# Performance work log

Measured on AMD Instinct MI355X. Metric: run time of the kernel, lower is better.

## Reference

```python
import jax, jax.numpy as jnp
import numpy as np

D_IN, D_HIDDEN, DT_RANK = 768, 16, 48


def setup_inputs() -> dict:
    key = jax.random.key(0)
    ks = jax.random.split(key, 6)
    b, l, d, n, r = 2, 2048, D_IN, D_HIDDEN, DT_RANK
    p = 3 * n + 2 * d + 2 * r  # x_proj output width = 1680
    x = jax.random.normal(ks[0], (b, l, d), jnp.float32)
    z = jax.random.normal(ks[1], (b, d, l), jnp.float32)
    # A_log = log(repeat(arange(1, n+1), 'n -> d n'))
    A_log = jnp.log(jnp.broadcast_to(jnp.arange(1, n + 1, dtype=jnp.float32), (d, n)))
    D = jnp.ones((d,), jnp.float32)
    W_xproj = jax.random.normal(ks[2], (p, d), jnp.float32) / np.sqrt(d)
    W_dt = jax.random.normal(ks[3], (d, r), jnp.float32) / np.sqrt(r)
    # dt bias init: inverse-softplus of dt ~ LogUniform(1e-3, 1e-1)
    dt = jnp.exp(jax.random.uniform(ks[4], (d,)) * (np.log(0.1) - np.log(0.001)) + np.log(0.001))
    dt = jnp.clip(dt, 1e-4)
    b_dt = dt + jnp.log(-jnp.expm1(-dt))
    return dict(x=x, z=z, A_log=A_log, D=D, W_xproj=W_xproj, W_dt=W_dt, b_dt=b_dt)


def reference(x, z, A_log, D, W_xproj, W_dt, b_dt):
    b, l, d = x.shape
    n = A_log.shape[1]
    r = W_dt.shape[1]
    A = -jnp.exp(A_log)                      # (d, n)
    proj = x @ W_xproj.T                     # (b, l, 3n + 2d + 2r)
    Bm = proj[..., :n]                       # (b, l, n)  input matrix B
    Cm = proj[..., 2 * n:3 * n]              # (b, l, n)  output matrix C
    dt = proj[..., 3 * n + 2 * d:3 * n + 2 * d + r]   # (b, l, r)
    # NOTE: source adds dt_proj bias via the Linear AND again via delta_bias -> 2*b_dt
    delta = jax.nn.softplus(dt @ W_dt.T + 2.0 * b_dt)  # (b, l, d)
    dA = jnp.exp(delta[..., None] * A)                  # (b, l, d, n)
    dBu = (delta * x)[..., None] * Bm[:, :, None, :]    # (b, l, d, n)

    def step(h, inp):
        dA_t, dBu_t, C_t = inp
        h = dA_t * h + dBu_t                 # (b, d, n)
        return h, jnp.einsum('bdn,bn->bd', h, C_t)

    h0 = jnp.zeros((b, d, n), x.dtype)
    _, ys = jax.lax.scan(step, h0, (jnp.swapaxes(dA, 0, 1), jnp.swapaxes(dBu, 0, 1), jnp.swapaxes(Cm, 0, 1)))
    y = jnp.swapaxes(ys, 0, 1) + x * D       # (b, l, d)  + skip D*u
    zl = jnp.swapaxes(z, 1, 2)               # z is (b, d, l) -> (b, l, d)
    return y * (zl * jax.nn.sigmoid(zl))     # gate with silu(z)
```

## Files before the change

kernel.cpp:

```cpp
#include <hip/hip_runtime.h>
#include <math.h>

#define BATCH 2
#define LSEQ  2048
#define DIM   768
#define NST   16
#define RDT   48
#define BL    (BATCH*LSEQ)
#define NCHUNK 32
#define CLEN   (LSEQ/NCHUNK)
#define CPAD   68
#define NPACK  (CLEN/4)
#define LP4    (LSEQ/4)
#define L2E    1.4426950408889634f

typedef __attribute__((ext_vector_type(8))) short short8;
typedef __attribute__((ext_vector_type(4))) float float4e;

__device__ __forceinline__ ushort f2bf(float f) {
    union { float f; unsigned u; } v; v.f = f;
    unsigned u = v.u;
    u += 0x7fffu + ((u >> 16) & 1u);
    return (ushort)(u >> 16);
}

template <int CTRL>
__device__ __forceinline__ float dpp_add(float v) {
    const int s = __builtin_amdgcn_update_dpp(__float_as_int(v), __float_as_int(v),
                                              CTRL, 0xF, 0xF, false);
    return v + __int_as_float(s);
}

__global__ __launch_bounds__(256) void pack_kernel(
        const float* __restrict__ x, const float* __restrict__ Wx,
        float* __restrict__ xT, ushort* __restrict__ Wbf) {
    if (blockIdx.y == DIM / 64) {
        const int blk = blockIdx.z * 32 + blockIdx.x;
        for (int idx = blk * 256 + threadIdx.x; idx < 80 * DIM; idx += 64 * 256) {
            const int j = idx / DIM;
            const int k = idx - j * DIM;
            const int row = (j < 16) ? j : ((j < 32) ? (j + 16) : (j + 1552));
            Wbf[idx] = f2bf(Wx[(size_t)row * DIM + k]);
        }
        return;
    }
    __shared__ float tile[64 * 65];
    const int r0 = blockIdx.x * 64;
    const int c0 = blockIdx.y * 64;
    const int b  = blockIdx.z;
    const int tid = threadIdx.x;
    {
        const int c4 = tid & 15, rb = tid >> 4;
        #pragma unroll
        for (int rr = 0; rr < 4; ++rr) {
            const int row = rr * 16 + rb;
            const float4 v = *(const float4*)(x + ((size_t)b * LSEQ + r0 + row) * DIM + c0 + c4 * 4);
            tile[(c4 * 4 + 0) * 65 + row] = v.x;
            tile[(c4 * 4 + 1) * 65 + row] = v.y;
            tile[(c4 * 4 + 2) * 65 + row] = v.z;
            tile[(c4 * 4 + 3) * 65 + row] = v.w;
        }
    }
    __syncthreads();
    {
        const int t4 = tid & 15, dq = tid >> 4;
        #pragma unroll
        for (int pass = 0; pass < 4; ++pass) {
            const int dd = pass * 16 + dq;
            float4 v;
            v.x = tile[dd * 65 + t4 * 4 + 0];
            v.y = tile[dd * 65 + t4 * 4 + 1];
            v.z = tile[dd * 65 + t4 * 4 + 2];
            v.w = tile[dd * 65 + t4 * 4 + 3];
            *(float4*)(xT + ((size_t)b * DIM + c0 + dd) * LSEQ + r0 + t4 * 4) = v;
        }
    }
}

__global__ __launch_bounds__(64) void proj_gemm_kernel(
        const float* __restrict__ x, const ushort* __restrict__ Wbf,
        float* __restrict__ Bpk, float* __restrict__ Cpk,
        float* __restrict__ dtpT) {
    const int m0   = blockIdx.x * 16;
    const int lane = threadIdx.x;
    const int col  = lane & 15;
    const int quad = lane >> 4;

    const float* A  = x + (size_t)(m0 + col) * DIM + quad * 8;
    const short* Bw = (const short*)Wbf;

    float4e acc[5] = {};
    #pragma unroll 4
    for (int kk = 0; kk < 24; ++kk) {
        const float4 a0 = *(const float4*)(A + kk * 32);
        const float4 a1 = *(const float4*)(A + kk * 32 + 4);
        short8 a;
        a[0] = (short)f2bf(a0.x); a[1] = (short)f2bf(a0.y);
        a[2] = (short)f2bf(a0.z); a[3] = (short)f2bf(a0.w);
        a[4] = (short)f2bf(a1.x); a[5] = (short)f2bf(a1.y);
        a[6] = (short)f2bf(a1.z); a[7] = (short)f2bf(a1.w);
        #pragma unroll
        for (int nt = 0; nt < 5; ++nt) {
            const short8 bf = *(const short8*)(Bw + (size_t)(nt * 16 + col) * DIM + kk * 32 + quad * 8);
            acc[nt] = __builtin_amdgcn_mfma_f32_16x16x32_bf16(a, bf, acc[nt], 0, 0, 0);
        }
    }

    const int b  = m0 >> 11;
    const int t0 = m0 & 2047;
    const size_t pk4 = ((size_t)(b * LP4 + (t0 >> 2) + quad)) * NST + col;
    ((float4*)Bpk)[pk4] = *(float4*)&acc[0];
    ((float4*)Cpk)[pk4] = *(float4*)&acc[1];
    #pragma unroll
    for (int nt = 2; nt < 5; ++nt) {
        const int r = (nt - 2) * 16 + col;
        *(float4*)(dtpT + ((size_t)(b * RDT + r)) * LSEQ + t0 + quad * 4) = *(float4*)&acc[nt];
    }
}

__global__ __launch_bounds__(256) void xpose_kernel(
        const float* __restrict__ in, float* __restrict__ out, int R, int C) {
    __shared__ float tile[64 * 65];
    const int r0 = blockIdx.x * 64;
    const int c0 = blockIdx.y * 64;
    const int b  = blockIdx.z;
    const int tid = threadIdx.x;
    {
        const int c4 = tid & 15, rb = tid >> 4;
        #pragma unroll
        for (int rr = 0; rr < 4; ++rr) {
            const int row = rr * 16 + rb;
            const float4 v = *(const float4*)(in + ((size_t)b * R + r0 + row) * C + c0 + c4 * 4);
            tile[(c4 * 4 + 0) * 65 + row] = v.x;
            tile[(c4 * 4 + 1) * 65 + row] = v.y;
            tile[(c4 * 4 + 2) * 65 + row] = v.z;
            tile[(c4 * 4 + 3) * 65 + row] = v.w;
        }
    }
    __syncthreads();
    {
        const int t4 = tid & 15, dq = tid >> 4;
        #pragma unroll
        for (int pass = 0; pass < 4; ++pass) {
            const int dd = pass * 16 + dq;
            float4 v;
            v.x = tile[dd * 65 + t4 * 4 + 0];
            v.y = tile[dd * 65 + t4 * 4 + 1];
            v.z = tile[dd * 65 + t4 * 4 + 2];
            v.w = tile[dd * 65 + t4 * 4 + 3];
            *(float4*)(out + ((size_t)b * C + c0 + dd) * R + r0 + t4 * 4) = v;
        }
    }
}

__global__ __launch_bounds__(512) void scan_kernel(
        const float* __restrict__ xT, const float* __restrict__ z,
        const float* __restrict__ A_log, const float* __restrict__ Dp,
        const float* __restrict__ Bpk, const float* __restrict__ Cpk,
        const float* __restrict__ dtpT, const float* __restrict__ Wdt,
        const float* __restrict__ bdt, float* __restrict__ yT) {
    __shared__ float sdel[NCHUNK * CPAD];
    __shared__ float sdlx[NCHUNK * CPAD];
    __shared__ float sx[NCHUNK * CPAD];
    __shared__ float sP[NCHUNK][NST];
    __shared__ float sq[NCHUNK][NST];
    __shared__ float sw[RDT];

    const int tid = threadIdx.x;
    const int ch = blockIdx.x;
    const int b = ch / DIM;
    const int d = ch % DIM;
    const size_t row = (size_t)ch * LSEQ;

    if (tid < RDT) sw[tid] = Wdt[(size_t)d * RDT + tid];
    const float4 xv4 = ((const float4*)(xT + row))[tid];
    ((float4*)sx)[(tid >> 4) * (CPAD / 4) + (tid & 15)] = xv4;
    __syncthreads();

    {
        const float bb = 2.0f * bdt[d];
        const float* dbase = dtpT + (size_t)b * RDT * LSEQ;
        float4 acc = make_float4(bb, bb, bb, bb);
        #pragma unroll 3
        for (int k4 = 0; k4 < RDT / 4; ++k4) {
            const float4 wv = ((const float4*)sw)[k4];
            #pragma unroll
            for (int j = 0; j < 4; ++j) {
                const int k = k4 * 4 + j;
                const float wk = (j == 0) ? wv.x : (j == 1) ? wv.y : (j == 2) ? wv.z : wv.w;
                const float4 v = ((const float4*)(dbase + (size_t)k * LSEQ))[tid];
                acc.x = fmaf(v.x, wk, acc.x);
                acc.y = fmaf(v.y, wk, acc.y);
                acc.z = fmaf(v.z, wk, acc.z);
                acc.w = fmaf(v.w, wk, acc.w);
            }
        }
        float4 sp;
        sp.x = (acc.x > 20.f) ? acc.x : __logf(1.f + __expf(acc.x));
        sp.y = (acc.y > 20.f) ? acc.y : __logf(1.f + __expf(acc.y));
        sp.z = (acc.z > 20.f) ? acc.z : __logf(1.f + __expf(acc.z));
        sp.w = (acc.w > 20.f) ? acc.w : __logf(1.f + __expf(acc.w));
        const int sidx = (tid >> 4) * (CPAD / 4) + (tid & 15);
        ((float4*)sdel)[sidx] = sp;
        ((float4*)sdlx)[sidx] = make_float4(sp.x * xv4.x, sp.y * xv4.y,
                                            sp.z * xv4.z, sp.w * xv4.w);
    }
    __syncthreads();

    const int g = tid >> 4;
    const int n = tid & 15;
    const float Aln2 = -__expf(A_log[d * NST + n]) * L2E;
    const float4* Bg = (const float4*)Bpk + ((size_t)(b * LP4 + g * NPACK) * NST + n);
    const float4* Cg = (const float4*)Cpk + ((size_t)(b * LP4 + g * NPACK) * NST + n);
    const float* dchunk  = sdel + g * CPAD;
    const float* uxchunk = sdlx + g * CPAD;

    {
        float h = 0.f, Ptot = 1.f;
        float4 Bn_ = Bg[0];
        #pragma unroll 4
        for (int p = 0; p < NPACK; ++p) {
            const float4 B4 = Bn_;
            if (p < NPACK - 1) Bn_ = Bg[(p + 1) * NST];
            const float4 dl = *(const float4*)(dchunk + 4 * p);
            const float4 ux = *(const float4*)(uxchunk + 4 * p);
            const float u0 = ux.x * B4.x, u1 = ux.y * B4.y;
            const float u2 = ux.z * B4.z, u3 = ux.w * B4.w;
            const float e0  = __builtin_amdgcn_exp2f(Aln2 * dl.x);
            const float dA1 = __builtin_amdgcn_exp2f(Aln2 * dl.y);
            const float dA2 = __builtin_amdgcn_exp2f(Aln2 * dl.z);
            const float dA3 = __builtin_amdgcn_exp2f(Aln2 * dl.w);
            float s = u0;
            s = fmaf(dA1, s, u1); s = fmaf(dA2, s, u2); s = fmaf(dA3, s, u3);
            const float E3 = ((e0 * dA1) * (dA2 * dA3));
            h = fmaf(E3, h, s);
            Ptot *= E3;
        }
        sP[g][n] = Ptot;
        sq[g][n] = h;
    }
    __syncthreads();

    {
        float Pc = sP[g][n], qc = sq[g][n];
        #pragma unroll
        for (int s = 1; s < NCHUNK; s <<= 1) {
            float Pp = 1.f, qp = 0.f;
            if (g >= s) { Pp = sP[g - s][n]; qp = sq[g - s][n]; }
            __syncthreads();
            qc = fmaf(Pc, qp, qc);
            Pc *= Pp;
            sP[g][n] = Pc; sq[g][n] = qc;
            __syncthreads();
        }
    }

    {
        float h = (g == 0) ? 0.f : sq[g - 1][n];
        float* ybuf = sdel;
        float4 Bn_ = Bg[0];
        float4 Cn_ = Cg[0];
        #pragma unroll 4
        for (int p = 0; p < NPACK; ++p) {
            const float4 B4 = Bn_, C4 = Cn_;
            if (p < NPACK - 1) { Bn_ = Bg[(p + 1) * NST]; Cn_ = Cg[(p + 1) * NST]; }
            const float4 dl = *(const float4*)(dchunk + 4 * p);
            const float4 ux = *(const float4*)(uxchunk + 4 * p);
            const float u0 = ux.x * B4.x, u1 = ux.y * B4.y;
            const float u2 = ux.z * B4.z, u3 = ux.w * B4.w;
            const float E0  = __builtin_amdgcn_exp2f(Aln2 * dl.x);
            const float dA1 = __builtin_amdgcn_exp2f(Aln2 * dl.y);
            const float dA2 = __builtin_amdgcn_exp2f(Aln2 * dl.z);
            const float dA3 = __builtin_amdgcn_exp2f(Aln2 * dl.w);
            const float E1 = E0 * dA1, E2 = E1 * dA2, E3 = E2 * dA3;
            const float s0 = u0;
            const float s1 = fmaf(dA1, s0, u1);
            const float s2 = fmaf(dA2, s1, u2);
            const float s3 = fmaf(dA3, s2, u3);
            const float h0 = fmaf(E0, h, s0);
            const float h1 = fmaf(E1, h, s1);
            const float h2 = fmaf(E2, h, s2);
            const float h3 = fmaf(E3, h, s3);
            h = h3;
            float p0 = h0 * C4.x, p1 = h1 * C4.y, p2 = h2 * C4.z, p3 = h3 * C4.w;
            p0 = dpp_add<0xB1>(p0); p0 = dpp_add<0x4E>(p0);
            p1 = dpp_add<0xB1>(p1); p1 = dpp_add<0x4E>(p1);
            p2 = dpp_add<0xB1>(p2); p2 = dpp_add<0x4E>(p2);
            p3 = dpp_add<0xB1>(p3); p3 = dpp_add<0x4E>(p3);
            float v = (n & 1) ? ((n & 2) ? p3 : p1) : ((n & 2) ? p2 : p0);
            v = dpp_add<0x124>(v);
            v = dpp_add<0x128>(v);
            if (n < 4) ybuf[g * CPAD + 4 * p + n] = v;
        }
    }
    __syncthreads();

    {
        const float Dd = Dp[d];
        const float* zrow = z + row;
        float* yrow = yT + row;
        const int t = tid * 4;
        const int idx = (t >> 6) * CPAD + (t & 63);
        const float4 yv = *(const float4*)(sdel + idx);
        const float4 xv = *(const float4*)(sx + idx);
        const float4 zv = ((const float4*)zrow)[tid];
        float4 o;
        o.x = fmaf(xv.x, Dd, yv.x) * zv.x / (1.f + __expf(-zv.x));
        o.y = fmaf(xv.y, Dd, yv.y) * zv.y / (1.f + __expf(-zv.y));
        o.z = fmaf(xv.z, Dd, yv.z) * zv.z / (1.f + __expf(-zv.z));
        o.w = fmaf(xv.w, Dd, yv.w) * zv.w / (1.f + __expf(-zv.w));
        ((float4*)yrow)[tid] = o;
    }
}

extern "C" void kernel_launch(void* const* d_in, const int* in_sizes, int n_in,
                              void* d_out, int out_size, void* d_ws, size_t ws_size,
                              hipStream_t stream) {
    const float* x     = (const float*)d_in[0];
    const float* z     = (const float*)d_in[1];
    const float* A_log = (const float*)d_in[2];
    const float* D     = (const float*)d_in[3];
    const float* Wx    = (const float*)d_in[4];
    const float* Wdt   = (const float*)d_in[5];
    const float* bdt   = (const float*)d_in[6];
    float* out = (float*)d_out;

    float* ws    = (float*)d_ws;
    float* Bpk   = ws;
    float* Cpk   = Bpk + (size_t)BATCH * LP4 * NST * 4;
    float* dtpT  = Cpk + (size_t)BATCH * LP4 * NST * 4;
    float* xT    = dtpT + (size_t)BATCH * RDT * LSEQ;
    float* yT    = xT;
    ushort* Wbf  = (ushort*)(xT + (size_t)BATCH * DIM * LSEQ);

    hipLaunchKernelGGL(pack_kernel, dim3(LSEQ / 64, DIM / 64 + 1, BATCH), dim3(256), 0, stream,
                       x, Wx, xT, Wbf);
    hipLaunchKernelGGL(proj_gemm_kernel, dim3(BL / 16), dim3(64), 0, stream,
                       x, Wbf, Bpk, Cpk, dtpT);
    hipLaunchKernelGGL(scan_kernel, dim3(BATCH * DIM), dim3(512), 0, stream,
                       xT, z, A_log, D, Bpk, Cpk, dtpT, Wdt, bdt, yT);
    hipLaunchKernelGGL(xpose_kernel, dim3(DIM / 64, LSEQ / 64, BATCH), dim3(256), 0, stream,
                       yT, out, DIM, LSEQ);
}
```

Measured before the change: 156.6 us.

## Split GEMM tiles across waves, halve scan chunks, fuse gating into transpose

Measured after the change: 165.2 us. 5.5% more time.

```diff
diff --git a/kernel.cpp b/kernel.cpp
--- a/kernel.cpp
+++ b/kernel.cpp
@@ -7,9 +7,8 @@
 #define NST   16
 #define RDT   48
 #define BL    (BATCH*LSEQ)
-#define NCHUNK 32
+#define NCHUNK 16
 #define CLEN   (LSEQ/NCHUNK)
-#define CPAD   68
 #define NPACK  (CLEN/4)
 #define LP4    (LSEQ/4)
 #define L2E    1.4426950408889634f
@@ -77,19 +76,20 @@
     }
 }
 
-__global__ __launch_bounds__(64) void proj_gemm_kernel(
+__global__ __launch_bounds__(320) void proj_gemm_kernel(
         const float* __restrict__ x, const ushort* __restrict__ Wbf,
         float* __restrict__ Bpk, float* __restrict__ Cpk,
         float* __restrict__ dtpT) {
     const int m0   = blockIdx.x * 16;
-    const int lane = threadIdx.x;
+    const int nt   = threadIdx.x >> 6;
+    const int lane = threadIdx.x & 63;
     const int col  = lane & 15;
     const int quad = lane >> 4;
 
     const float* A  = x + (size_t)(m0 + col) * DIM + quad * 8;
-    const short* Bw = (const short*)Wbf;
-
-    float4e acc[5] = {};
+    const short* Bw = (const short*)Wbf + (size_t)(nt * 16 + col) * DIM + quad * 8;
+
+    float4e acc = {};
     #pragma unroll 4
     for (int kk = 0; kk < 24; ++kk) {
         const float4 a0 = *(const float4*)(A + kk * 32);
@@ -99,69 +99,29 @@
         a[2] = (short)f2bf(a0.z); a[3] = (short)f2bf(a0.w);
         a[4] = (short)f2bf(a1.x); a[5] = (short)f2bf(a1.y);
         a[6] = (short)f2bf(a1.z); a[7] = (short)f2bf(a1.w);
-        #pragma unroll
-        for (int nt = 0; nt < 5; ++nt) {
-            const short8 bf = *(const short8*)(Bw + (size_t)(nt * 16 + col) * DIM + kk * 32 + quad * 8);
-            acc[nt] = __builtin_amdgcn_mfma_f32_16x16x32_bf16(a, bf, acc[nt], 0, 0, 0);
-        }
+        const short8 bf = *(const short8*)(Bw + kk * 32);
+        acc = __builtin_amdgcn_mfma_f32_16x16x32_bf16(a, bf, acc, 0, 0, 0);
     }
 
     const int b  = m0 >> 11;
     const int t0 = m0 & 2047;
-    const size_t pk4 = ((size_t)(b * LP4 + (t0 >> 2) + quad)) * NST + col;
-    ((float4*)Bpk)[pk4] = *(float4*)&acc[0];
-    ((float4*)Cpk)[pk4] = *(float4*)&acc[1];
-    #pragma unroll
-    for (int nt = 2; nt < 5; ++nt) {
+    if (nt == 0) {
+        ((float4*)Bpk)[((size_t)(b * LP4 + (t0 >> 2) + quad)) * NST + col] = *(float4*)&acc;
+    } else if (nt == 1) {
+        ((float4*)Cpk)[((size_t)(b * LP4 + (t0 >> 2) + quad)) * NST + col] = *(float4*)&acc;
+    } else {
         const int r = (nt - 2) * 16 + col;
-        *(float4*)(dtpT + ((size_t)(b * RDT + r)) * LSEQ + t0 + quad * 4) = *(float4*)&acc[nt];
-    }
-}
-
-__global__ __launch_bounds__(256) void xpose_kernel(
-        const float* __restrict__ in, float* __restrict__ out, int R, int C) {
-    __shared__ float tile[64 * 65];
-    const int r0 = blockIdx.x * 64;
-    const int c0 = blockIdx.y * 64;
-    const int b  = blockIdx.z;
-    const int tid = threadIdx.x;
-    {
-        const int c4 = tid & 15, rb = tid >> 4;
-        #pragma unroll
-        for (int rr = 0; rr < 4; ++rr) {
-            const int row = rr * 16 + rb;
-            const float4 v = *(const float4*)(in + ((size_t)b * R + r0 + row) * C + c0 + c4 * 4);
-            tile[(c4 * 4 + 0) * 65 + row] = v.x;
-            tile[(c4 * 4 + 1) * 65 + row] = v.y;
-            tile[(c4 * 4 + 2) * 65 + row] = v.z;
-            tile[(c4 * 4 + 3) * 65 + row] = v.w;
-        }
-    }
-    __syncthreads();
-    {
-        const int t4 = tid & 15, dq = tid >> 4;
-        #pragma unroll
-        for (int pass = 0; pass < 4; ++pass) {
-            const int dd = pass * 16 + dq;
-            float4 v;
-            v.x = tile[dd * 65 + t4 * 4 + 0];
-            v.y = tile[dd * 65 + t4 * 4 + 1];
-            v.z = tile[dd * 65 + t4 * 4 + 2];
-            v.w = tile[dd * 65 + t4 * 4 + 3];
-            *(float4*)(out + ((size_t)b * C + c0 + dd) * R + r0 + t4 * 4) = v;
-        }
-    }
-}
-
-__global__ __launch_bounds__(512) void scan_kernel(
-        const float* __restrict__ xT, const float* __restrict__ z,
-        const float* __restrict__ A_log, const float* __restrict__ Dp,
+        *(float4*)(dtpT + ((size_t)(b * RDT + r)) * LSEQ + t0 + quad * 4) = *(float4*)&acc;
+    }
+}
+
+__global__ __launch_bounds__(256) void scan_kernel(
+        const float* __restrict__ xT, const float* __restrict__ A_log,
+        const float* __restrict__ Dp,
         const float* __restrict__ Bpk, const float* __restrict__ Cpk,
         const float* __restrict__ dtpT, const float* __restrict__ Wdt,
-        const float* __restrict__ bdt, float* __restrict__ yT) {
-    __shared__ float sdel[NCHUNK * CPAD];
-    __shared__ float sdlx[NCHUNK * CPAD];
-    __shared__ float sx[NCHUNK * CPAD];
+        const float* __restrict__ bdt, float* __restrict__ yv) {
+    __shared__ float sdel[LSEQ];
     __shared__ float sP[NCHUNK][NST];
     __shared__ float sq[NCHUNK][NST];
     __shared__ float sw[RDT];
@@ -173,37 +133,36 @@
     const size_t row = (size_t)ch * LSEQ;
 
     if (tid < RDT) sw[tid] = Wdt[(size_t)d * RDT + tid];
-    const float4 xv4 = ((const float4*)(xT + row))[tid];
-    ((float4*)sx)[(tid >> 4) * (CPAD / 4) + (tid & 15)] = xv4;
     __syncthreads();
 
     {
         const float bb = 2.0f * bdt[d];
         const float* dbase = dtpT + (size_t)b * RDT * LSEQ;
-        float4 acc = make_float4(bb, bb, bb, bb);
-        #pragma unroll 3
-        for (int k4 = 0; k4 < RDT / 4; ++k4) {
-            const float4 wv = ((const float4*)sw)[k4];
-            #pragma unroll
-            for (int j = 0; j < 4; ++j) {
-                const int k = k4 * 4 + j;
-                const float wk = (j == 0) ? wv.x : (j == 1) ? wv.y : (j == 2) ? wv.z : wv.w;
-                const float4 v = ((const float4*)(dbase + (size_t)k * LSEQ))[tid];
-                acc.x = fmaf(v.x, wk, acc.x);
-                acc.y = fmaf(v.y, wk, acc.y);
-                acc.z = fmaf(v.z, wk, acc.z);
-                acc.w = fmaf(v.w, wk, acc.w);
+        #pragma unroll
+        for (int i = 0; i < 2; ++i) {
+            const int idx = tid + 256 * i;
+            float4 acc = make_float4(bb, bb, bb, bb);
+            #pragma unroll 3
+            for (int k4 = 0; k4 < RDT / 4; ++k4) {
+                const float4 wv = ((const float4*)sw)[k4];
+                #pragma unroll
+                for (int j = 0; j < 4; ++j) {
+                    const int k = k4 * 4 + j;
+                    const float wk = (j == 0) ? wv.x : (j == 1) ? wv.y : (j == 2) ? wv.z : wv.w;
+                    const float4 v = ((const float4*)(dbase + (size_t)k * LSEQ))[idx];
+                    acc.x = fmaf(v.x, wk, acc.x);
+                    acc.y = fmaf(v.y, wk, acc.y);
+                    acc.z = fmaf(v.z, wk, acc.z);
+                    acc.w = fmaf(v.w, wk, acc.w);
+                }
             }
-        }
-        float4 sp;
-        sp.x = (acc.x > 20.f) ? acc.x : __logf(1.f + __expf(acc.x));
-        sp.y = (acc.y > 20.f) ? acc.y : __logf(1.f + __expf(acc.y));
-        sp.z = (acc.z > 20.f) ? acc.z : __logf(1.f + __expf(acc.z));
-        sp.w = (acc.w > 20.f) ? acc.w : __logf(1.f + __expf(acc.w));
-        const int sidx = (tid >> 4) * (CPAD / 4) + (tid & 15);
-        ((float4*)sdel)[sidx] = sp;
-        ((float4*)sdlx)[sidx] = make_float4(sp.x * xv4.x, sp.y * xv4.y,
-                                            sp.z * xv4.z, sp.w * xv4.w);
+            float4 sp;
+            sp.x = (acc.x > 20.f) ? acc.x : __logf(1.f + __expf(acc.x));
+            sp.y = (acc.y > 20.f) ? acc.y : __logf(1.f + __expf(acc.y));
+            sp.z = (acc.z > 20.f) ? acc.z : __logf(1.f + __expf(acc.z));
+            sp.w = (acc.w > 20.f) ? acc.w : __logf(1.f + __expf(acc.w));
+            ((float4*)sdel)[idx] = sp;
+        }
     }
     __syncthreads();
 
@@ -212,20 +171,18 @@
     const float Aln2 = -__expf(A_log[d * NST + n]) * L2E;
     const float4* Bg = (const float4*)Bpk + ((size_t)(b * LP4 + g * NPACK) * NST + n);
     const float4* Cg = (const float4*)Cpk + ((size_t)(b * LP4 + g * NPACK) * NST + n);
-    const float* dchunk  = sdel + g * CPAD;
-    const float* uxchunk = sdlx + g * CPAD;
+    const float4* xr = (const float4*)(xT + row) + g * NPACK;
 
     {
         float h = 0.f, Ptot = 1.f;
-        float4 Bn_ = Bg[0];
+        float4 Bn_ = Bg[0], xn_ = xr[0];
         #pragma unroll 4
         for (int p = 0; p < NPACK; ++p) {
-            const float4 B4 = Bn_;
-            if (p < NPACK - 1) Bn_ = Bg[(p + 1) * NST];
-            const float4 dl = *(const float4*)(dchunk + 4 * p);
-            const float4 ux = *(const float4*)(uxchunk + 4 * p);
-            const float u0 = ux.x * B4.x, u1 = ux.y * B4.y;
-            const float u2 = ux.z * B4.z, u3 = ux.w * B4.w;
+            const float4 B4 = Bn_, x4 = xn_;
+            if (p < NPACK - 1) { Bn_ = Bg[(p + 1) * NST]; xn_ = xr[p + 1]; }
+            const float4 dl = ((const float4*)sdel)[g * NPACK + p];
+            const float u0 = dl.x * x4.x * B4.x, u1 = dl.y * x4.y * B4.y;
+            const float u2 = dl.z * x4.z * B4.z, u3 = dl.w * x4.w * B4.w;
             const float e0  = __builtin_amdgcn_exp2f(Aln2 * dl.x);
             const float dA1 = __builtin_amdgcn_exp2f(Aln2 * dl.y);
             const float dA2 = __builtin_amdgcn_exp2f(Aln2 * dl.z);
@@ -257,17 +214,15 @@
 
     {
         float h = (g == 0) ? 0.f : sq[g - 1][n];
-        float* ybuf = sdel;
-        float4 Bn_ = Bg[0];
-        float4 Cn_ = Cg[0];
+        const float Dd = Dp[d];
+        float4 Bn_ = Bg[0], Cn_ = Cg[0], xn_ = xr[0];
         #pragma unroll 4
         for (int p = 0; p < NPACK; ++p) {
-            const float4 B4 = Bn_, C4 = Cn_;
-            if (p < NPACK - 1) { Bn_ = Bg[(p + 1) * NST]; Cn_ = Cg[(p + 1) * NST]; }
-            const float4 dl = *(const float4*)(dchunk + 4 * p);
-            const float4 ux = *(const float4*)(uxchunk + 4 * p);
-            const float u0 = ux.x * B4.x, u1 = ux.y * B4.y;
-            const float u2 = ux.z * B4.z, u3 = ux.w * B4.w;
+            const float4 B4 = Bn_, C4 = Cn_, x4 = xn_;
+            if (p < NPACK - 1) { Bn_ = Bg[(p + 1) * NST]; Cn_ = Cg[(p + 1) * NST]; xn_ = xr[p + 1]; }
+            const float4 dl = ((const float4*)sdel)[g * NPACK + p];
+            const float u0 = dl.x * x4.x * B4.x, u1 = dl.y * x4.y * B4.y;
+            const float u2 = dl.z * x4.z * B4.z, u3 = dl.w * x4.w * B4.w;
             const float E0  = __builtin_amdgcn_exp2f(Aln2 * dl.x);
             const float dA1 = __builtin_amdgcn_exp2f(Aln2 * dl.y);
             const float dA2 = __builtin_amdgcn_exp2f(Aln2 * dl.z);
@@ -290,26 +245,49 @@
             float v = (n & 1) ? ((n & 2) ? p3 : p1) : ((n & 2) ? p2 : p0);
             v = dpp_add<0x124>(v);
             v = dpp_add<0x128>(v);
-            if (n < 4) ybuf[g * CPAD + 4 * p + n] = v;
-        }
-    }
-    __syncthreads();
-
-    {
-        const float Dd = Dp[d];
-        const float* zrow = z + row;
-        float* yrow = yT + row;
-        const int t = tid * 4;
-        const int idx = (t >> 6) * CPAD + (t & 63);
-        const float4 yv = *(const float4*)(sdel + idx);
-        const float4 xv = *(const float4*)(sx + idx);
-        const float4 zv = ((const float4*)zrow)[tid];
-        float4 o;
-        o.x = fmaf(xv.x, Dd, yv.x) * zv.x / (1.f + __expf(-zv.x));
-        o.y = fmaf(xv.y, Dd, yv.y) * zv.y / (1.f + __expf(-zv.y));
-        o.z = fmaf(xv.z, Dd, yv.z) * zv.z / (1.f + __expf(-zv.z));
-        o.w = fmaf(xv.w, Dd, yv.w) * zv.w / (1.f + __expf(-zv.w));
-        ((float4*)yrow)[tid] = o;
+            if (n < 4) {
+                const float xc = (n == 0) ? x4.x : (n == 1) ? x4.y : (n == 2) ? x4.z : x4.w;
+                yv[row + g * CLEN + 4 * p + n] = fmaf(xc, Dd, v);
+            }
+        }
+    }
+}
+
+__global__ __launch_bounds__(256) void xpose_out_kernel(
+        const float* __restrict__ yv, const float* __restrict__ z,
+        float* __restrict__ out) {
+    __shared__ float tile[64 * 65];
+    const int r0 = blockIdx.x * 64;
+    const int c0 = blockIdx.y * 64;
+    const int b  = blockIdx.z;
+    const int tid = threadIdx.x;
+    {
+        const int c4 = tid & 15, rb = tid >> 4;
+        #pragma unroll
+        for (int rr = 0; rr < 4; ++rr) {
+            const int row = rr * 16 + rb;
+            const size_t gidx = ((size_t)b * DIM + r0 + row) * LSEQ + c0 + c4 * 4;
+            const float4 v = *(const float4*)(yv + gidx);
+            const float4 zv = *(const float4*)(z + gidx);
+            tile[(c4 * 4 + 0) * 65 + row] = v.x * zv.x / (1.f + __expf(-zv.x));
+            tile[(c4 * 4 + 1) * 65 + row] = v.y * zv.y / (1.f + __expf(-zv.y));
+            tile[(c4 * 4 + 2) * 65 + row] = v.z * zv.z / (1.f + __expf(-zv.z));
+            tile[(c4 * 4 + 3) * 65 + row] = v.w * zv.w / (1.f + __expf(-zv.w));
+        }
+    }
+    __syncthreads();
+    {
+        const int t4 = tid & 15, dq = tid >> 4;
+        #pragma unroll
+        for (int pass = 0; pass < 4; ++pass) {
+            const int ll = pass * 16 + dq;
+            float4 v;
+            v.x = tile[ll * 65 + t4 * 4 + 0];
+            v.y = tile[ll * 65 + t4 * 4 + 1];
+            v.z = tile[ll * 65 + t4 * 4 + 2];
+            v.w = tile[ll * 65 + t4 * 4 + 3];
+            *(float4*)(out + ((size_t)b * LSEQ + c0 + ll) * DIM + r0 + t4 * 4) = v;
+        }
     }
 }
 
@@ -330,15 +308,15 @@
     float* Cpk   = Bpk + (size_t)BATCH * LP4 * NST * 4;
     float* dtpT  = Cpk + (size_t)BATCH * LP4 * NST * 4;
     float* xT    = dtpT + (size_t)BATCH * RDT * LSEQ;
-    float* yT    = xT;
+    float* yv    = xT;
     ushort* Wbf  = (ushort*)(xT + (size_t)BATCH * DIM * LSEQ);
 
     hipLaunchKernelGGL(pack_kernel, dim3(LSEQ / 64, DIM / 64 + 1, BATCH), dim3(256), 0, stream,
                        x, Wx, xT, Wbf);
-    hipLaunchKernelGGL(proj_gemm_kernel, dim3(BL / 16), dim3(64), 0, stream,
+    hipLaunchKernelGGL(proj_gemm_kernel, dim3(BL / 16), dim3(320), 0, stream,
                        x, Wbf, Bpk, Cpk, dtpT);
-    hipLaunchKernelGGL(scan_kernel, dim3(BATCH * DIM), dim3(512), 0, stream,
-                       xT, z, A_log, D, Bpk, Cpk, dtpT, Wdt, bdt, yT);
-    hipLaunchKernelGGL(xpose_kernel, dim3(DIM / 64, LSEQ / 64, BATCH), dim3(256), 0, stream,
-                       yT, out, DIM, LSEQ);
-}
+    hipLaunchKernelGGL(scan_kernel, dim3(BATCH * DIM), dim3(256), 0, stream,
+                       xT, A_log, D, Bpk, Cpk, dtpT, Wdt, bdt, yv);
+    hipLaunchKernelGGL(xpose_out_kernel, dim3(DIM / 64, LSEQ / 64, BATCH), dim3(256), 0, stream,
+                       yv, z, out);
+}
```
